# Optimization experiments

Measured on AMD Instinct MI355X. Metric: run time of the kernel, lower is better.

Reference implementation:

```python
import jax, jax.numpy as jnp
import numpy as np

B, S, E, N, H = 2, 2048, 2048, 16, 128  # batch, seq, embed, heads, depth


def sine_table(features, length, min_timescale=1.0, max_timescale=10000.0):
    fraction = jnp.arange(0, features, 2, dtype=jnp.float32) / features
    timescale = min_timescale * (max_timescale / min_timescale) ** fraction
    sinusoid_inp = jnp.einsum('i,j->ij', jnp.arange(length, dtype=jnp.float32), 1.0 / timescale,
                              precision=jax.lax.Precision.HIGHEST)
    sinusoid_inp = jnp.concatenate([sinusoid_inp, sinusoid_inp], axis=-1)  # [L, features]
    return jnp.sin(sinusoid_inp), jnp.cos(sinusoid_inp)


def rotate_half(x):
    x1, x2 = jnp.split(x, 2, axis=-1)
    return jnp.concatenate([-x2, x1], axis=-1)


def apply_rotary(q, k, cos, sin):
    # q: [B,S,N,H], k: [B,T,N,H]; cos/sin: [L,H] broadcast over (seq, depth)
    qcos = cos[: q.shape[1]][None, :, None, :]
    qsin = sin[: q.shape[1]][None, :, None, :]
    kcos = cos[: k.shape[1]][None, :, None, :]
    ksin = sin[: k.shape[1]][None, :, None, :]
    return q * qcos + rotate_half(q) * qsin, k * kcos + rotate_half(k) * ksin


def setup_inputs() -> dict:
    key = jax.random.key(0)
    ks = jax.random.split(key, 6)
    scale = 1.0 / np.sqrt(E)
    return {
        'x_q': jax.random.normal(ks[0], (B, S, E), jnp.float32),
        'x_kv': jax.random.normal(ks[1], (B, S, E), jnp.float32),
        'WQ': jax.random.normal(ks[2], (E, N, H), jnp.float32) * scale,
        'WK': jax.random.normal(ks[3], (E, N, H), jnp.float32) * scale,
        'WV': jax.random.normal(ks[4], (E, N, H), jnp.float32) * scale,
        'WO': jax.random.normal(ks[5], (N, H, E), jnp.float32) * scale,
    }


def reference(x_q, x_kv, WQ, WK, WV, WO):
    q = jnp.einsum('bse,enh->bsnh', x_q, WQ)
    k = jnp.einsum('bte,enh->btnh', x_kv, WK)
    v = jnp.einsum('bte,enh->btnh', x_kv, WV)

    sin, cos = sine_table(q.shape[-1], max(q.shape[1], k.shape[1]))
    q, k = apply_rotary(q, k, cos, sin)

    # causal attention bias: [1,1,S,T]
    s_len, t_len = q.shape[1], k.shape[1]
    causal = jnp.arange(s_len)[:, None] >= jnp.arange(t_len)[None, :]
    bias = jnp.where(causal, 0.0, -1e10).astype(jnp.float32)[None, None]

    logits = jnp.einsum('bsnh,btnh->bnst', q, k) / np.sqrt(H) + bias
    probs = jax.nn.softmax(logits, axis=-1)
    a = jnp.einsum('bnst,btnh->bsnh', probs, v)
    o = jnp.einsum('bsnh,nhe->bse', a, WO)
    return o
```

## Files before the change

kernel.cpp:

```cpp
#include <hip/hip_runtime.h>
#include <hip/hip_bf16.h>

typedef __bf16 bf16;
typedef __attribute__((ext_vector_type(8))) __bf16 bf16x8;
typedef __attribute__((ext_vector_type(4))) __bf16 bf16x4;
typedef __attribute__((ext_vector_type(4))) float f32x4;

typedef const __attribute__((address_space(1))) void* gptr_t;
typedef __attribute__((address_space(3))) void* sptr_t;

__device__ __forceinline__ void gload16(const void* g, void* l) {
  __builtin_amdgcn_global_load_lds((gptr_t)g, (sptr_t)l, 16, 0, 0);
}

#define MFMA_BF16(a, b, c) __builtin_amdgcn_mfma_f32_16x16x32_bf16((a), (b), (c), 0, 0, 0)

namespace {
constexpr int kB = 2, kS = 2048, kE = 2048, kN = 16, kH = 128;
constexpr int kBS = kB * kS;
constexpr int kNH = kN * kH;
constexpr float kScale = 0.08838834764831845f;
constexpr float kLog2e = 1.4426950408889634f;
}

__global__ void k_cvt(const float* __restrict__ in, bf16* __restrict__ out) {
  int i = blockIdx.x * 256 + threadIdx.x;
  float4 v = reinterpret_cast<const float4*>(in)[i];
  bf16x4 o = { (bf16)v.x, (bf16)v.y, (bf16)v.z, (bf16)v.w };
  reinterpret_cast<bf16x4*>(out)[i] = o;
}

__global__ void k_tconv(const float* __restrict__ in, bf16* __restrict__ out) {
  __shared__ bf16 tile[64][66];
  int bx = blockIdx.x & 31, by = blockIdx.x >> 5;
  int r0 = by * 64, c0 = bx * 64;
  int t = threadIdx.x;
  int c = t & 63, rb = t >> 6;
#pragma unroll
  for (int j = 0; j < 16; ++j) {
    int r = rb + j * 4;
    tile[r][c] = (bf16)in[(size_t)(r0 + r) * 2048 + c0 + c];
  }
  __syncthreads();
  int rr = t & 63;
#pragma unroll
  for (int j = 0; j < 16; ++j) {
    int cc = rb + j * 4;
    out[(size_t)(c0 + cc) * 2048 + r0 + rr] = tile[rr][cc];
  }
}

__global__ void k_vtrans(const bf16* __restrict__ V, bf16* __restrict__ Vt) {
  __shared__ bf16 tile[64][66];
  int bid = blockIdx.x;
  int bn = bid >> 6;
  int s0 = ((bid >> 1) & 31) * 64;
  int h0 = (bid & 1) * 64;
  size_t base = (size_t)bn * kS * kH;
  int t = threadIdx.x, c = t & 63, rb = t >> 6;
#pragma unroll
  for (int j = 0; j < 16; ++j) {
    int r = rb + j * 4;
    tile[r][c] = V[base + (size_t)(s0 + r) * kH + h0 + c];
  }
  __syncthreads();
#pragma unroll
  for (int j = 0; j < 16; ++j) {
    int hh = rb + j * 4;
    Vt[base + (size_t)(h0 + hh) * kS + s0 + (t & 63)] = tile[t & 63][hh];
  }
}

__global__ void k_rope(bf16* __restrict__ Qd, bf16* __restrict__ Kd) {
  int tid = blockIdx.x * 256 + threadIdx.x;
  int i = tid & 63;
  int s = (tid >> 6) & (kS - 1);
  int bn = tid >> 17;
  size_t base = ((size_t)bn * kS + s) * kH;
  float inv = exp2f(-(float)i * 0.20762050593046457f);
  float ang = (float)s * inv;
  float sn, cs;
  sincosf(ang, &sn, &cs);
  float q1 = (float)Qd[base + i], q2 = (float)Qd[base + i + 64];
  Qd[base + i]      = (bf16)(q1 * cs - q2 * sn);
  Qd[base + i + 64] = (bf16)(q2 * cs + q1 * sn);
  float k1 = (float)Kd[base + i], k2 = (float)Kd[base + i + 64];
  Kd[base + i]      = (bf16)(k1 * cs - k2 * sn);
  Kd[base + i + 64] = (bf16)(k2 * cs + k1 * sn);
}

template <int MODE>
__global__ __launch_bounds__(256, 2) void k_gemm(const bf16* __restrict__ A,
                                                 const bf16* __restrict__ Bt,
                                                 void* __restrict__ Cout) {
  constexpr int Kk = 2048;
  __shared__ __align__(16) bf16 As[128][32];
  __shared__ __align__(16) bf16 Bs[128][32];
  int bid = blockIdx.x;
  int swz = (bid & 7) * 64 + (bid >> 3);
  int mt = swz >> 4, nt = swz & 15;
  int m0 = mt * 128, n0 = nt * 128;
  int t = threadIdx.x, wid = t >> 6, lane = t & 63;
  int l16 = lane & 15, lq = lane >> 4;
  int wr = wid >> 1, wc = wid & 1;
  f32x4 acc[4][4] = {};

  for (int kt = 0; kt < Kk / 32; ++kt) {
    int k0 = kt * 32;
#pragma unroll
    for (int i = 0; i < 2; ++i) {
      int idx = i * 256 + t;
      const bf16* ga = A + (size_t)(m0 + (idx >> 2)) * Kk + k0 + (idx & 3) * 8;
      gload16(ga, (char*)(&As[0][0]) + i * 4096 + wid * 1024);
      const bf16* gb = Bt + (size_t)(n0 + (idx >> 2)) * Kk + k0 + (idx & 3) * 8;
      gload16(gb, (char*)(&Bs[0][0]) + i * 4096 + wid * 1024);
    }
    __syncthreads();
    bf16x8 af[4], bfr[4];
#pragma unroll
    for (int mi = 0; mi < 4; ++mi)
      af[mi] = *(const bf16x8*)&As[wr * 64 + mi * 16 + l16][lq * 8];
#pragma unroll
    for (int ni = 0; ni < 4; ++ni)
      bfr[ni] = *(const bf16x8*)&Bs[wc * 64 + ni * 16 + l16][lq * 8];
#pragma unroll
    for (int mi = 0; mi < 4; ++mi)
#pragma unroll
      for (int ni = 0; ni < 4; ++ni)
        acc[mi][ni] = MFMA_BF16(af[mi], bfr[ni], acc[mi][ni]);
    __syncthreads();
  }

#pragma unroll
  for (int mi = 0; mi < 4; ++mi) {
    int mrow_base = m0 + wr * 64 + mi * 16 + lq * 4;
#pragma unroll
    for (int ni = 0; ni < 4; ++ni) {
      int col = n0 + wc * 64 + ni * 16 + l16;
#pragma unroll
      for (int r = 0; r < 4; ++r) {
        int mrow = mrow_base + r;
        float v = acc[mi][ni][r];
        if (MODE == 0) {
          int b = mrow >> 11, s = mrow & 2047, n = col >> 7, h = col & 127;
          ((bf16*)Cout)[(((size_t)(b * kN + n) * kS + s)) * kH + h] = (bf16)v;
        } else {
          ((float*)Cout)[(size_t)mrow * 2048 + col] = v;
        }
      }
    }
  }
}

__global__ __launch_bounds__(256, 2) void k_attn(const bf16* __restrict__ Q,
                                                 const bf16* __restrict__ Kg,
                                                 const bf16* __restrict__ Vt,
                                                 bf16* __restrict__ AO) {
  __shared__ __align__(16) bf16 Ks[64 * 128];
  __shared__ __align__(16) bf16 Vs[128 * 64];
  __shared__ __align__(16) bf16 Ps[4][32][72];
  int bid = blockIdx.x;
  int bn = bid >> 4;
  int qt = bid & 15;
  int q0 = qt * 128;
  int t = threadIdx.x, wid = t >> 6, lane = t & 63;
  int l16 = lane & 15, lq = lane >> 4;
  size_t bnSH = (size_t)bn * kS * kH;

  bf16x8 qf[2][4];
#pragma unroll
  for (int mi = 0; mi < 2; ++mi)
#pragma unroll
    for (int ks = 0; ks < 4; ++ks) {
      int row = q0 + wid * 32 + mi * 16 + l16;
      qf[mi][ks] = *(const bf16x8*)(Q + bnSH + (size_t)row * kH + ks * 32 + lq * 8);
    }

  f32x4 oacc[2][8] = {};
  float mrun[2][4], lrun[2][4];
#pragma unroll
  for (int mi = 0; mi < 2; ++mi)
#pragma unroll
    for (int r = 0; r < 4; ++r) { mrun[mi][r] = -1e30f; lrun[mi][r] = 0.f; }

  int ntiles = (q0 + 128) >> 6;
  for (int kt = 0; kt < ntiles; ++kt) {
    int kv0 = kt * 64;
#pragma unroll
    for (int i = 0; i < 4; ++i) {
      int idx = i * 256 + t;
      {
        int row = idx >> 4, ch = idx & 15;
        int gch = ch ^ (row & 7);
        gload16(Kg + bnSH + (size_t)(kv0 + row) * kH + gch * 8,
                (char*)Ks + i * 4096 + wid * 1024);
      }
      {
        int row = idx >> 3, ch = idx & 7;
        int gch = ch ^ (row & 7);
        gload16(Vt + bnSH + (size_t)row * kS + kv0 + gch * 8,
                (char*)Vs + i * 4096 + wid * 1024);
      }
    }
    __syncthreads();

    f32x4 sacc[2][4] = {};
#pragma unroll
    for (int ks = 0; ks < 4; ++ks) {
#pragma unroll
      for (int ni = 0; ni < 4; ++ni) {
        int sp = ni * 16 + l16;
        int hb = (ks * 32 + lq * 8) * 2;
        bf16x8 kb = *(const bf16x8*)((const char*)Ks + sp * 256 + (hb ^ ((sp & 7) << 4)));
        sacc[0][ni] = MFMA_BF16(qf[0][ks], kb, sacc[0][ni]);
        sacc[1][ni] = MFMA_BF16(qf[1][ks], kb, sacc[1][ni]);
      }
    }

    bool need_mask = (kv0 + 63) > q0;
#pragma unroll
    for (int mi = 0; mi < 2; ++mi)
#pragma unroll
      for (int ni = 0; ni < 4; ++ni) {
        f32x4 v = sacc[mi][ni] * kScale;
        if (need_mask) {
#pragma unroll
          for (int r = 0; r < 4; ++r) {
            int qrow = q0 + wid * 32 + mi * 16 + lq * 4 + r;
            int col = kv0 + ni * 16 + l16;
            if (col > qrow) v[r] = -1e30f;
          }
        }
        sacc[mi][ni] = v;
      }

#pragma unroll
    for (int mi = 0; mi < 2; ++mi)
#pragma unroll
      for (int r = 0; r < 4; ++r) {
        float pm = fmaxf(fmaxf(sacc[mi][0][r], sacc[mi][1][r]),
                         fmaxf(sacc[mi][2][r], sacc[mi][3][r]));
        pm = fmaxf(pm, __shfl_xor(pm, 1));
        pm = fmaxf(pm, __shfl_xor(pm, 2));
        pm = fmaxf(pm, __shfl_xor(pm, 4));
        pm = fmaxf(pm, __shfl_xor(pm, 8));
        float mold = mrun[mi][r];
        float mnew = fmaxf(mold, pm);
        float alpha = exp2f((mold - mnew) * kLog2e);
        mrun[mi][r] = mnew;
        float rs = 0.f;
#pragma unroll
        for (int ni = 0; ni < 4; ++ni) {
          float p = exp2f((sacc[mi][ni][r] - mnew) * kLog2e);
          sacc[mi][ni][r] = p;
          rs += p;
        }
        rs += __shfl_xor(rs, 1);
        rs += __shfl_xor(rs, 2);
        rs += __shfl_xor(rs, 4);
        rs += __shfl_xor(rs, 8);
        lrun[mi][r] = lrun[mi][r] * alpha + rs;
#pragma unroll
        for (int nj = 0; nj < 8; ++nj) oacc[mi][nj][r] *= alpha;
      }

#pragma unroll
    for (int mi = 0; mi < 2; ++mi)
#pragma unroll
      for (int ni = 0; ni < 4; ++ni)
#pragma unroll
        for (int r = 0; r < 4; ++r)
          Ps[wid][mi * 16 + lq * 4 + r][ni * 16 + l16] = (bf16)sacc[mi][ni][r];

#pragma unroll
    for (int ks = 0; ks < 2; ++ks) {
      bf16x8 pa0 = *(const bf16x8*)&Ps[wid][l16][ks * 32 + lq * 8];
      bf16x8 pa1 = *(const bf16x8*)&Ps[wid][16 + l16][ks * 32 + lq * 8];
#pragma unroll
      for (int nj = 0; nj < 8; ++nj) {
        int h = nj * 16 + l16;
        int sb = (ks * 64 + lq * 16) ^ ((h & 7) << 4);
        bf16x8 vb = *(const bf16x8*)((const char*)Vs + h * 128 + sb);
        oacc[0][nj] = MFMA_BF16(pa0, vb, oacc[0][nj]);
        oacc[1][nj] = MFMA_BF16(pa1, vb, oacc[1][nj]);
      }
    }
    __syncthreads();
  }

  int b = bn >> 4, n = bn & 15;
#pragma unroll
  for (int mi = 0; mi < 2; ++mi)
#pragma unroll
    for (int r = 0; r < 4; ++r) {
      float inv = 1.0f / lrun[mi][r];
      int qrow = q0 + wid * 32 + mi * 16 + lq * 4 + r;
#pragma unroll
      for (int nj = 0; nj < 8; ++nj) {
        float v = oacc[mi][nj][r] * inv;
        AO[(((size_t)b * kS + qrow) * kN + n) * kH + nj * 16 + l16] = (bf16)v;
      }
    }
}

extern "C" void kernel_launch(void* const* d_in, const int* in_sizes, int n_in,
                              void* d_out, int out_size, void* d_ws, size_t ws_size,
                              hipStream_t stream) {
  (void)in_sizes; (void)n_in; (void)out_size; (void)ws_size;
  const float* x_q  = (const float*)d_in[0];
  const float* x_kv = (const float*)d_in[1];
  const float* WQ   = (const float*)d_in[2];
  const float* WK   = (const float*)d_in[3];
  const float* WV   = (const float*)d_in[4];
  const float* WO   = (const float*)d_in[5];
  float* out = (float*)d_out;
  char* w = (char*)d_ws;
  const size_t MB = 1ull << 20;
  bf16* xq  = (bf16*)(w + 0 * MB);
  bf16* xkv = (bf16*)(w + 16 * MB);
  bf16* WqT = (bf16*)(w + 32 * MB);
  bf16* WkT = (bf16*)(w + 40 * MB);
  bf16* WvT = (bf16*)(w + 48 * MB);
  bf16* WoT = (bf16*)(w + 56 * MB);
  bf16* Qb  = (bf16*)(w + 64 * MB);
  bf16* Kb  = (bf16*)(w + 80 * MB);
  bf16* Vb  = (bf16*)(w + 96 * MB);
  bf16* AO  = xq;
  bf16* Vtb = xkv;

  k_cvt<<<8192, 256, 0, stream>>>(x_q, xq);
  k_cvt<<<8192, 256, 0, stream>>>(x_kv, xkv);
  k_tconv<<<1024, 256, 0, stream>>>(WQ, WqT);
  k_tconv<<<1024, 256, 0, stream>>>(WK, WkT);
  k_tconv<<<1024, 256, 0, stream>>>(WV, WvT);
  k_tconv<<<1024, 256, 0, stream>>>(WO, WoT);
  k_gemm<0><<<512, 256, 0, stream>>>(xq,  WqT, Qb);
  k_gemm<0><<<512, 256, 0, stream>>>(xkv, WkT, Kb);
  k_gemm<0><<<512, 256, 0, stream>>>(xkv, WvT, Vb);
  k_rope<<<16384, 256, 0, stream>>>(Qb, Kb);
  k_vtrans<<<2048, 256, 0, stream>>>(Vb, Vtb);
  k_attn<<<512, 256, 0, stream>>>(Qb, Kb, Vtb, AO);
  k_gemm<1><<<512, 256, 0, stream>>>(AO, WoT, out);
}
```

Measured before the change: 521.7 us.

## Use 8 waves of 16 query rows each in attention and balance causal tiles

The attention kernel now runs 512 threads per block, with each wave owning 16 query rows instead of 32, which halves per-thread accumulator registers and allows more resident waves. The causal mask check becomes per wave, so more waves skip masking. Block indices are remapped so the second half of the grid walks query tiles in reverse order, pairing long and short causal workloads across the dispatch. In exchange, each wave issues half as many MFMAs per K/V tile load and LDS fragment read, which lowers reuse of the shared K and V tiles.

```diff
diff --git a/kernel.cpp b/kernel.cpp
--- a/kernel.cpp
+++ b/kernel.cpp
@@ -152,59 +152,55 @@
   }
 }
 
-__global__ __launch_bounds__(256, 2) void k_attn(const bf16* __restrict__ Q,
+__global__ __launch_bounds__(512, 4) void k_attn(const bf16* __restrict__ Q,
                                                  const bf16* __restrict__ Kg,
                                                  const bf16* __restrict__ Vt,
                                                  bf16* __restrict__ AO) {
   __shared__ __align__(16) bf16 Ks[64 * 128];
   __shared__ __align__(16) bf16 Vs[128 * 64];
-  __shared__ __align__(16) bf16 Ps[4][32][72];
+  __shared__ __align__(16) bf16 Ps[8][16][72];
   int bid = blockIdx.x;
-  int bn = bid >> 4;
-  int qt = bid & 15;
+  int half = bid >> 8;
+  int bn = (half << 4) | ((bid >> 4) & 15);
+  int qt = (bid & 15) ^ (half ? 15 : 0);
   int q0 = qt * 128;
   int t = threadIdx.x, wid = t >> 6, lane = t & 63;
   int l16 = lane & 15, lq = lane >> 4;
   size_t bnSH = (size_t)bn * kS * kH;
 
-  bf16x8 qf[2][4];
-#pragma unroll
-  for (int mi = 0; mi < 2; ++mi)
-#pragma unroll
-    for (int ks = 0; ks < 4; ++ks) {
-      int row = q0 + wid * 32 + mi * 16 + l16;
-      qf[mi][ks] = *(const bf16x8*)(Q + bnSH + (size_t)row * kH + ks * 32 + lq * 8);
-    }
-
-  f32x4 oacc[2][8] = {};
-  float mrun[2][4], lrun[2][4];
-#pragma unroll
-  for (int mi = 0; mi < 2; ++mi)
-#pragma unroll
-    for (int r = 0; r < 4; ++r) { mrun[mi][r] = -1e30f; lrun[mi][r] = 0.f; }
+  int qrow_a = q0 + wid * 16 + l16;
+  bf16x8 qf[4];
+#pragma unroll
+  for (int ks = 0; ks < 4; ++ks)
+    qf[ks] = *(const bf16x8*)(Q + bnSH + (size_t)qrow_a * kH + ks * 32 + lq * 8);
+
+  f32x4 oacc[8] = {};
+  float mrun[4], lrun[4];
+#pragma unroll
+  for (int r = 0; r < 4; ++r) { mrun[r] = -1e30f; lrun[r] = 0.f; }
 
   int ntiles = (q0 + 128) >> 6;
   for (int kt = 0; kt < ntiles; ++kt) {
     int kv0 = kt * 64;
 #pragma unroll
-    for (int i = 0; i < 4; ++i) {
-      int idx = i * 256 + t;
+    for (int i = 0; i < 2; ++i) {
+      int idx = i * 512 + t;
       {
         int row = idx >> 4, ch = idx & 15;
         int gch = ch ^ (row & 7);
         gload16(Kg + bnSH + (size_t)(kv0 + row) * kH + gch * 8,
-                (char*)Ks + i * 4096 + wid * 1024);
+                (char*)Ks + i * 8192 + wid * 1024);
       }
       {
         int row = idx >> 3, ch = idx & 7;
         int gch = ch ^ (row & 7);
         gload16(Vt + bnSH + (size_t)row * kS + kv0 + gch * 8,
-                (char*)Vs + i * 4096 + wid * 1024);
+                (char*)Vs + i * 8192 + wid * 1024);
       }
     }
     __syncthreads();
 
-    f32x4 sacc[2][4] = {};
+    f32x4 sacc[4] = {};
 #pragma unroll
     for (int ks = 0; ks < 4; ++ks) {
 #pragma unroll
@@ -212,77 +208,68 @@
         int sp = ni * 16 + l16;
         int hb = (ks * 32 + lq * 8) * 2;
         bf16x8 kb = *(const bf16x8*)((const char*)Ks + sp * 256 + (hb ^ ((sp & 7) << 4)));
-        sacc[0][ni] = MFMA_BF16(qf[0][ks], kb, sacc[0][ni]);
-        sacc[1][ni] = MFMA_BF16(qf[1][ks], kb, sacc[1][ni]);
-      }
-    }
-
-    bool need_mask = (kv0 + 63) > q0;
-#pragma unroll
-    for (int mi = 0; mi < 2; ++mi)
+        sacc[ni] = MFMA_BF16(qf[ks], kb, sacc[ni]);
+      }
+    }
+
+    bool need_mask = (kv0 + 63) > (q0 + wid * 16);
+#pragma unroll
+    for (int ni = 0; ni < 4; ++ni) {
+      f32x4 v = sacc[ni] * kScale;
+      if (need_mask) {
+#pragma unroll
+        for (int r = 0; r < 4; ++r) {
+          int qrow = q0 + wid * 16 + lq * 4 + r;
+          int col = kv0 + ni * 16 + l16;
+          if (col > qrow) v[r] = -1e30f;
+        }
+      }
+      sacc[ni] = v;
+    }
+
+#pragma unroll
+    for (int r = 0; r < 4; ++r) {
+      float pm = fmaxf(fmaxf(sacc[0][r], sacc[1][r]),
+                       fmaxf(sacc[2][r], sacc[3][r]));
+      pm = fmaxf(pm, __shfl_xor(pm, 1));
+      pm = fmaxf(pm, __shfl_xor(pm, 2));
+      pm = fmaxf(pm, __shfl_xor(pm, 4));
+      pm = fmaxf(pm, __shfl_xor(pm, 8));
+      float mold = mrun[r];
+      float mnew = fmaxf(mold, pm);
+      float alpha = exp2f((mold - mnew) * kLog2e);
+      mrun[r] = mnew;
+      float rs = 0.f;
 #pragma unroll
       for (int ni = 0; ni < 4; ++ni) {
-        f32x4 v = sacc[mi][ni] * kScale;
-        if (need_mask) {
-#pragma unroll
-          for (int r = 0; r < 4; ++r) {
-            int qrow = q0 + wid * 32 + mi * 16 + lq * 4 + r;
-            int col = kv0 + ni * 16 + l16;
-            if (col > qrow) v[r] = -1e30f;
-          }
-        }
-        sacc[mi][ni] = v;
-      }
-
-#pragma unroll
-    for (int mi = 0; mi < 2; ++mi)
-#pragma unroll
-      for (int r = 0; r < 4; ++r) {
-        float pm = fmaxf(fmaxf(sacc[mi][0][r], sacc[mi][1][r]),
-                         fmaxf(sacc[mi][2][r], sacc[mi][3][r]));
-        pm = fmaxf(pm, __shfl_xor(pm, 1));
-        pm = fmaxf(pm, __shfl_xor(pm, 2));
-        pm = fmaxf(pm, __shfl_xor(pm, 4));
-        pm = fmaxf(pm, __shfl_xor(pm, 8));
-        float mold = mrun[mi][r];
-        float mnew = fmaxf(mold, pm);
-        float alpha = exp2f((mold - mnew) * kLog2e);
-        mrun[mi][r] = mnew;
-        float rs = 0.f;
-#pragma unroll
-        for (int ni = 0; ni < 4; ++ni) {
-          float p = exp2f((sacc[mi][ni][r] - mnew) * kLog2e);
-          sacc[mi][ni][r] = p;
-          rs += p;
-        }
-        rs += __shfl_xor(rs, 1);
-        rs += __shfl_xor(rs, 2);
-        rs += __shfl_xor(rs, 4);
-        rs += __shfl_xor(rs, 8);
-        lrun[mi][r] = lrun[mi][r] * alpha + rs;
-#pragma unroll
-        for (int nj = 0; nj < 8; ++nj) oacc[mi][nj][r] *= alpha;
-      }
-
-#pragma unroll
-    for (int mi = 0; mi < 2; ++mi)
-#pragma unroll
-      for (int ni = 0; ni < 4; ++ni)
-#pragma unroll
-        for (int r = 0; r < 4; ++r)
-          Ps[wid][mi * 16 + lq * 4 + r][ni * 16 + l16] = (bf16)sacc[mi][ni][r];
+        float p = exp2f((sacc[ni][r] - mnew) * kLog2e);
+        sacc[ni][r] = p;
+        rs += p;
+      }
+      rs += __shfl_xor(rs, 1);
+      rs += __shfl_xor(rs, 2);
+      rs += __shfl_xor(rs, 4);
+      rs += __shfl_xor(rs, 8);
+      lrun[r] = lrun[r] * alpha + rs;
+#pragma unroll
+      for (int nj = 0; nj < 8; ++nj) oacc[nj][r] *= alpha;
+    }
+
+#pragma unroll
+    for (int ni = 0; ni < 4; ++ni)
+#pragma unroll
+      for (int r = 0; r < 4; ++r)
+        Ps[wid][lq * 4 + r][ni * 16 + l16] = (bf16)sacc[ni][r];
 
 #pragma unroll
     for (int ks = 0; ks < 2; ++ks) {
-      bf16x8 pa0 = *(const bf16x8*)&Ps[wid][l16][ks * 32 + lq * 8];
-      bf16x8 pa1 = *(const bf16x8*)&Ps[wid][16 + l16][ks * 32 + lq * 8];
+      bf16x8 pa = *(const bf16x8*)&Ps[wid][l16][ks * 32 + lq * 8];
 #pragma unroll
       for (int nj = 0; nj < 8; ++nj) {
         int h = nj * 16 + l16;
         int sb = (ks * 64 + lq * 16) ^ ((h & 7) << 4);
         bf16x8 vb = *(const bf16x8*)((const char*)Vs + h * 128 + sb);
-        oacc[0][nj] = MFMA_BF16(pa0, vb, oacc[0][nj]);
-        oacc[1][nj] = MFMA_BF16(pa1, vb, oacc[1][nj]);
+        oacc[nj] = MFMA_BF16(pa, vb, oacc[nj]);
       }
     }
     __syncthreads();
@@ -290,17 +277,15 @@
 
   int b = bn >> 4, n = bn & 15;
 #pragma unroll
-  for (int mi = 0; mi < 2; ++mi)
-#pragma unroll
-    for (int r = 0; r < 4; ++r) {
-      float inv = 1.0f / lrun[mi][r];
-      int qrow = q0 + wid * 32 + mi * 16 + lq * 4 + r;
-#pragma unroll
-      for (int nj = 0; nj < 8; ++nj) {
-        float v = oacc[mi][nj][r] * inv;
-        AO[(((size_t)b * kS + qrow) * kN + n) * kH + nj * 16 + l16] = (bf16)v;
-      }
-    }
+  for (int r = 0; r < 4; ++r) {
+    float inv = 1.0f / lrun[r];
+    int qrow = q0 + wid * 16 + lq * 4 + r;
+#pragma unroll
+    for (int nj = 0; nj < 8; ++nj) {
+      float v = oacc[nj][r] * inv;
+      AO[(((size_t)b * kS + qrow) * kN + n) * kH + nj * 16 + l16] = (bf16)v;
+    }
+  }
 }
 
 extern "C" void kernel_launch(void* const* d_in, const int* in_sizes, int n_in,
@@ -339,6 +324,6 @@
   k_gemm<0><<<512, 256, 0, stream>>>(xkv, WvT, Vb);
   k_rope<<<16384, 256, 0, stream>>>(Qb, Kb);
   k_vtrans<<<2048, 256, 0, stream>>>(Vb, Vtb);
-  k_attn<<<512, 256, 0, stream>>>(Qb, Kb, Vtb, AO);
+  k_attn<<<512, 512, 0, stream>>>(Qb, Kb, Vtb, AO);
   k_gemm<1><<<512, 256, 0, stream>>>(AO, WoT, out);
 }
```

Result: faster. 471.5 us (-9.6%).
